# Performance work log

Measured on AMD Instinct MI355X. Metric: run time of the kernel, lower is better.

Reference implementation:

```python
import jax, jax.numpy as jnp
import numpy as np
import math

B, S, HID, H = 2, 2048, 2048, 16
D = HID // H  # head_dim = 128


def rotate_half(x):
    x1, x2 = x[..., : x.shape[-1] // 2], x[..., x.shape[-1] // 2:]
    return jnp.concatenate((-x2, x1), axis=-1)


def setup_inputs() -> dict:
    key = jax.random.key(0)
    ks = jax.random.split(key, 6)
    x = jax.random.normal(ks[0], (B, S, HID), dtype=jnp.float32)
    # learned projection weights (torch Linear: y = x @ W.T); store as [in, out]
    scale = 1.0 / math.sqrt(HID)
    Wq = jax.random.normal(ks[1], (HID, HID), dtype=jnp.float32) * scale
    Wk = jax.random.normal(ks[2], (HID, HID), dtype=jnp.float32) * scale
    Wv = jax.random.normal(ks[3], (HID, HID), dtype=jnp.float32) * scale
    Wo = jax.random.normal(ks[4], (HID, HID), dtype=jnp.float32) * scale
    # causal additive mask [1,1,S,S]
    causal = jnp.tril(jnp.ones((S, S), dtype=bool))
    attention_mask = jnp.where(causal, 0.0, -1e9).astype(jnp.float32)[None, None]
    # ALiBi bias: slope per head times key position, broadcast over queries
    slopes = 2.0 ** (-8.0 * (jnp.arange(1, H + 1, dtype=jnp.float32) / H))
    alibi = (-slopes[:, None] * jnp.arange(S, dtype=jnp.float32)[None, :])[None, :, None, :]  # [1,H,1,S]
    # RoPE tables broadcastable to [B,H,S,D]
    inv_freq = 1.0 / (10000.0 ** (jnp.arange(0, D // 2, dtype=jnp.float32) / (D // 2)))
    t = jnp.arange(S, dtype=jnp.float32)
    freqs = t[:, None] * inv_freq[None, :]            # [S, D/2]
    emb = jnp.concatenate((freqs, freqs), axis=-1)    # [S, D]
    freqs_cos = jnp.cos(emb)[None, None]              # [1,1,S,D]
    freqs_sin = jnp.sin(emb)[None, None]
    return {"x": x, "Wq": Wq, "Wk": Wk, "Wv": Wv, "Wo": Wo,
            "attention_mask": attention_mask, "alibi": alibi,
            "freqs_cos": freqs_cos, "freqs_sin": freqs_sin}


def reference(x, Wq, Wk, Wv, Wo, attention_mask, alibi, freqs_cos, freqs_sin):
    b, s, _ = x.shape
    def split_heads(y):
        return y.reshape(b, s, H, D).transpose(0, 2, 1, 3)  # [B,H,S,D]
    q = split_heads(x @ Wq)
    k = split_heads(x @ Wk)
    v = split_heads(x @ Wv)
    q = q * freqs_cos + rotate_half(q) * freqs_sin
    k = k * freqs_cos + rotate_half(k) * freqs_sin
    scores = jnp.einsum('bhqd,bhkd->bhqk', q, k) / math.sqrt(D)
    scores = scores + attention_mask + alibi
    attn = jax.nn.softmax(scores, axis=-1)  # dropout p=0 (eval) -> identity
    out = jnp.einsum('bhqk,bhkd->bhqd', attn, v)
    out = out.transpose(0, 2, 1, 3).reshape(b, s, HID)
    return out @ Wo
```

## Files before the change

kernel.cpp:

```cpp
#include <hip/hip_runtime.h>

#define S_LEN   2048
#define HEADS   16
#define HID_DIM 2048
#define HEAD_D  128
#define BATCH   2

typedef __bf16          bf16x8 __attribute__((ext_vector_type(8)));
typedef unsigned short  u16x8  __attribute__((ext_vector_type(8)));
typedef unsigned short  u16x4  __attribute__((ext_vector_type(4)));
typedef float           f32x4  __attribute__((ext_vector_type(4)));

__device__ __forceinline__ unsigned short f2bf(float f) {
  unsigned u = __builtin_bit_cast(unsigned, f);
  u += 0x7FFFu + ((u >> 16) & 1u);
  return (unsigned short)(u >> 16);
}
__device__ __forceinline__ float bf2f(unsigned short s) {
  unsigned u = ((unsigned)s) << 16;
  return __builtin_bit_cast(float, u);
}

__device__ __forceinline__ f32x4 mfma16(u16x8 a, u16x8 b, f32x4 c) {
  return __builtin_amdgcn_mfma_f32_16x16x32_bf16(
      __builtin_bit_cast(bf16x8, a), __builtin_bit_cast(bf16x8, b), c, 0, 0, 0);
}

__device__ __forceinline__ void async_load16(const void* g, void* l) {
  __builtin_amdgcn_global_load_lds(
      (const __attribute__((address_space(1))) void*)g,
      (__attribute__((address_space(3))) void*)l, 16, 0, 0);
}

__global__ __launch_bounds__(256) void cvt_bf16(const float* __restrict__ in,
                                                unsigned short* __restrict__ out,
                                                int n8) {
  for (int i = blockIdx.x * blockDim.x + threadIdx.x; i < n8;
       i += gridDim.x * blockDim.x) {
    const float4* p = (const float4*)in + 2L * i;
    float4 a = p[0], b = p[1];
    u16x8 v;
    v[0] = f2bf(a.x); v[1] = f2bf(a.y); v[2] = f2bf(a.z); v[3] = f2bf(a.w);
    v[4] = f2bf(b.x); v[5] = f2bf(b.y); v[6] = f2bf(b.z); v[7] = f2bf(b.w);
    ((u16x8*)out)[i] = v;
  }
}

__global__ __launch_bounds__(256) void transpose_cvt3(
    const float* __restrict__ W0, const float* __restrict__ W1,
    const float* __restrict__ W2, unsigned short* __restrict__ O0,
    unsigned short* __restrict__ O1, unsigned short* __restrict__ O2,
    int dim) {
  __shared__ float tile[32][33];
  const int z = blockIdx.z;
  const float* W = (z == 0) ? W0 : (z == 1) ? W1 : W2;
  unsigned short* Wt = (z == 0) ? O0 : (z == 1) ? O1 : O2;
  const int bx = blockIdx.x * 32, by = blockIdx.y * 32;
  const int tx = threadIdx.x, ty = threadIdx.y;
#pragma unroll
  for (int i = 0; i < 32; i += 8)
    tile[ty + i][tx] = W[(long)(by + ty + i) * dim + bx + tx];
  __syncthreads();
#pragma unroll
  for (int i = 0; i < 32; i += 8)
    Wt[(long)(bx + ty + i) * dim + by + tx] = f2bf(tile[tx][ty + i]);
}

__global__ __launch_bounds__(256) void transpose_cvt(const float* __restrict__ W,
                                                     unsigned short* __restrict__ Wt,
                                                     int dim) {
  __shared__ float tile[32][33];
  const int bx = blockIdx.x * 32, by = blockIdx.y * 32;
  const int tx = threadIdx.x, ty = threadIdx.y;
#pragma unroll
  for (int i = 0; i < 32; i += 8)
    tile[ty + i][tx] = W[(long)(by + ty + i) * dim + bx + tx];
  __syncthreads();
#pragma unroll
  for (int i = 0; i < 32; i += 8)
    Wt[(long)(bx + ty + i) * dim + by + tx] = f2bf(tile[tx][ty + i]);
}

__global__ __launch_bounds__(256) void transpose_v(const unsigned short* __restrict__ V,
                                                   unsigned short* __restrict__ Vt) {
  __shared__ unsigned short tile[32][34];
  const int s0 = blockIdx.x * 32, d0 = blockIdx.y * 32, bh = blockIdx.z;
  const int b = bh >> 4, h = bh & 15;
  const int tx = threadIdx.x, ty = threadIdx.y;
#pragma unroll
  for (int i = 0; i < 32; i += 8)
    tile[ty + i][tx] =
        V[(long)(b * S_LEN + s0 + ty + i) * HID_DIM + h * HEAD_D + d0 + tx];
  __syncthreads();
#pragma unroll
  for (int i = 0; i < 32; i += 8)
    Vt[((long)bh * HEAD_D + d0 + ty + i) * S_LEN + s0 + tx] = tile[tx][ty + i];
}

__global__ __launch_bounds__(256) void rope_qk(unsigned short* __restrict__ Qb,
                                               unsigned short* __restrict__ Kb,
                                               const float* __restrict__ fcos,
                                               const float* __restrict__ fsin) {
  const long i = (long)blockIdx.x * blockDim.x + threadIdx.x;
  const int d = (int)(i & 63);
  const int h = (int)((i >> 6) & (HEADS - 1));
  const long row = i >> 10;
  const int s = (int)(row & (S_LEN - 1));
  const long base = row * HID_DIM + h * HEAD_D + d;
  const float c0 = fcos[s * HEAD_D + d], c1 = fcos[s * HEAD_D + d + 64];
  const float s0 = fsin[s * HEAD_D + d], s1 = fsin[s * HEAD_D + d + 64];
  const float q0 = bf2f(Qb[base]), q1 = bf2f(Qb[base + 64]);
  Qb[base]      = f2bf(q0 * c0 - q1 * s0);
  Qb[base + 64] = f2bf(q1 * c1 + q0 * s1);
  const float k0 = bf2f(Kb[base]), k1 = bf2f(Kb[base + 64]);
  Kb[base]      = f2bf(k0 * c0 - k1 * s0);
  Kb[base + 64] = f2bf(k1 * c1 + k0 * s1);
}

template <int BM>
__global__ __launch_bounds__(512, 2) void gemm9(
    const unsigned short* __restrict__ A,
    const unsigned short* __restrict__ Bt0,
    unsigned short* __restrict__ Cb0,
    float* __restrict__ Cf,
    int M, int N, int K, long zsB, long zsC) {
  constexpr int MF = BM / 32;
  constexpr int AR = BM / 128;
  constexpr int TR = AR + 2;
  __shared__ __align__(16) unsigned short Abuf[4][BM * 32];
  __shared__ __align__(16) unsigned short Bbuf[4][256 * 32];
  const int t = threadIdx.x;
  const int lane = t & 63;
  const int w = t >> 6;
  const int wr = w >> 2, wc = w & 3;
  const int l15 = lane & 15, l4 = lane >> 4;

  const int nwg = gridDim.x;
  const int bid = blockIdx.x;
  const int sw = (bid & 7) * (nwg >> 3) + (bid >> 3);
  const int nbx = N >> 8, nby = M / BM;
  const int z = sw / (nbx * nby);
  const int rem = sw - z * nbx * nby;
  const int by = rem / nbx;
  const int bx = rem - by * nbx;

  const unsigned short* Bt = Bt0 + (long)z * zsB;
  unsigned short* Cb = Cb0 ? Cb0 + (long)z * zsC : nullptr;

  f32x4 acc[MF][4] = {};

  const int kcol = 8 * ((t & 3) ^ ((t >> 3) & 3));
  const unsigned short* aSrc = A + ((long)by * BM + (t >> 2)) * K + kcol;
  const unsigned short* bSrc = Bt + ((long)bx * 256 + (t >> 2)) * K + kcol;

  const int swzr = 8 * (l4 ^ ((l15 >> 1) & 3));
  const int aROff = (wr * (BM / 2) + l15) * 32 + swzr;
  const int bROff = (wc * 64 + l15) * 32 + swzr;

  const int NT = K >> 5;

#define STG(slot, kt_) do {                                              \
    _Pragma("unroll")                                                    \
    for (int r_ = 0; r_ < AR; ++r_)                                      \
      async_load16(aSrc + (long)(kt_) * 32 + (long)r_ * 128 * K,         \
                   (char*)(&Abuf[slot][0]) + r_ * 8192 + t * 16);        \
    async_load16(bSrc + (long)(kt_) * 32,                                \
                 (char*)(&Bbuf[slot][0]) + t * 16);                      \
    async_load16(bSrc + (long)(kt_) * 32 + 128L * K,                     \
                 (char*)(&Bbuf[slot][0]) + 8192 + t * 16);               \
  } while (0)

  STG(0, 0);
  STG(1, 1);
  asm volatile("s_waitcnt vmcnt(%0)" ::"n"(TR) : "memory");
  __builtin_amdgcn_s_barrier();

  for (int kt = 0; kt < NT; ++kt) {
    const int slot = kt & 3;
    const unsigned short* Ab = &Abuf[slot][0];
    const unsigned short* Bb = &Bbuf[slot][0];
    const bool stg = (kt + 2) < NT;
    u16x8 af[MF], bfr[4];
#pragma unroll
    for (int n = 0; n < 4; ++n) bfr[n] = *(const u16x8*)&Bb[bROff + n * 512];
#pragma unroll
    for (int m = 0; m < MF; ++m) af[m] = *(const u16x8*)&Ab[aROff + m * 512];
    if (stg) STG((kt + 2) & 3, kt + 2);
    __builtin_amdgcn_s_setprio(1);
#pragma unroll
    for (int m = 0; m < MF; ++m)
#pragma unroll
      for (int n = 0; n < 4; ++n)
        acc[m][n] = mfma16(af[m], bfr[n], acc[m][n]);
    __builtin_amdgcn_s_setprio(0);
    __builtin_amdgcn_sched_barrier(0);
    if (kt + 1 < NT) {
      if (stg) asm volatile("s_waitcnt vmcnt(%0)" ::"n"(TR) : "memory");
      else     asm volatile("s_waitcnt vmcnt(0)" ::: "memory");
      __builtin_amdgcn_s_barrier();
    }
  }
#undef STG

  const long orow = (long)by * BM + wr * (BM / 2) + l4 * 4;
  const long ocol = (long)bx * 256 + wc * 64 + l15;
#pragma unroll
  for (int m = 0; m < MF; ++m)
#pragma unroll
    for (int n = 0; n < 4; ++n)
#pragma unroll
      for (int r = 0; r < 4; ++r) {
        const long row = orow + m * 16 + r;
        const long col = ocol + n * 16;
        if (Cb) Cb[row * N + col] = f2bf(acc[m][n][r]);
        else    Cf[row * N + col] = acc[m][n][r];
      }
}

__global__ __launch_bounds__(256) void attn_fwd5(const unsigned short* __restrict__ Q,
                                                 const unsigned short* __restrict__ K,
                                                 const unsigned short* __restrict__ Vt,
                                                 const float* __restrict__ alibi,
                                                 unsigned short* __restrict__ O) {
  __shared__ __align__(16) unsigned short Kl[2][32 * 128];
  __shared__ __align__(16) unsigned short Vl[2][64 * 64];
  __shared__ __align__(16) unsigned short Pl[4][32][40];
  const int t = threadIdx.x;
  const int lane = t & 63;
  const int w = t >> 6;
  const int l15 = lane & 15, l4 = lane >> 4;

  const int bid = blockIdx.x;
  const int xcd = bid & 7;
  const int idx = bid >> 3;
  const int qh = idx >> 4;
  const int ql = idx & 15;
  const int qt = (qh < 2) ? ql : (15 - ql);
  const int bh = xcd * 4 + qh;
  const int b = bh >> 4, h = bh & 15;
  const int q0b = qt * 128;
  const int q0 = q0b + w * 32;
  const float nslope = alibi[h * S_LEN + 1];
  const float scale = 0.08838834764831845f;

  const long rowbase = ((long)b * S_LEN) * HID_DIM + h * HEAD_D;
  const long vtbase  = ((long)bh * HEAD_D) * S_LEN;

  u16x8 qf[2][4];
  {
    const unsigned short* qp = Q + rowbase + (long)(q0 + l15) * HID_DIM + l4 * 8;
#pragma unroll
    for (int m = 0; m < 2; ++m)
#pragma unroll
      for (int ds = 0; ds < 4; ++ds)
        qf[m][ds] = *(const u16x8*)(qp + (long)m * 16 * HID_DIM + ds * 32);
  }

  f32x4 acc[2][8] = {};
  float m_r[2] = {-1e30f, -1e30f};
  float l_r[2] = {0.f, 0.f};

  int dd, rw, cbl;
  dd = 16 * t;        rw = dd >> 8; cbl = (dd & 255) ^ ((rw & 7) << 4);
  const unsigned short* ksrc0 = K + rowbase + (long)rw * HID_DIM + (cbl >> 1);
  dd = 4096 + 16 * t; rw = dd >> 8; cbl = (dd & 255) ^ ((rw & 7) << 4);
  const unsigned short* ksrc1 = K + rowbase + (long)rw * HID_DIM + (cbl >> 1);
  dd = 16 * t;        rw = dd >> 7; cbl = (dd & 127) ^ ((rw & 3) << 4);
  const unsigned short* vsrc0 =
      Vt + vtbase + (long)(2 * rw + (cbl >> 6)) * S_LEN + ((cbl & 63) >> 1);
  dd = 4096 + 16 * t; rw = dd >> 7; cbl = (dd & 127) ^ ((rw & 3) << 4);
  const unsigned short* vsrc1 =
      Vt + vtbase + (long)(2 * rw + (cbl >> 6)) * S_LEN + ((cbl & 63) >> 1);

#define ASTAGE(buf, kt_) do {                                             \
    const long kadd = (long)(kt_) * 32 * HID_DIM;                         \
    async_load16(ksrc0 + kadd, (char*)(&Kl[buf][0]) + 16 * t);            \
    async_load16(ksrc1 + kadd, (char*)(&Kl[buf][0]) + 4096 + 16 * t);     \
    async_load16(vsrc0 + (kt_) * 32, (char*)(&Vl[buf][0]) + 16 * t);      \
    async_load16(vsrc1 + (kt_) * 32, (char*)(&Vl[buf][0]) + 4096 + 16 * t); \
  } while (0)

  const int ntB = qt * 4 + 4;
  const int mykt = q0 >> 5;

  ASTAGE(0, 0);
  __syncthreads();

  int cur = 0;
  for (int kt = 0; kt < ntB; ++kt) {
    const int kb = kt * 32;
    if (kt + 1 < ntB) ASTAGE(cur ^ 1, kt + 1);
    if (kt <= mykt) {
      const char* Kc = (const char*)&Kl[cur][0];
      const char* Vc = (const char*)&Vl[cur][0];
      f32x4 sacc[2][2] = {};
#pragma unroll
      for (int ds = 0; ds < 4; ++ds) {
        u16x8 kfr[2];
#pragma unroll
        for (int n = 0; n < 2; ++n) {
          const int R = 16 * n + l15;
          const int cb = (ds * 64 + l4 * 16) ^ ((l15 & 7) << 4);
          kfr[n] = *(const u16x8*)(Kc + R * 256 + cb);
        }
#pragma unroll
        for (int n = 0; n < 2; ++n)
#pragma unroll
          for (int m = 0; m < 2; ++m)
            sacc[n][m] = mfma16(kfr[n], qf[m][ds], sacc[n][m]);
      }
#pragma unroll
      for (int m = 0; m < 2; ++m) {
        const int q = q0 + 16 * m + l15;
        float pv[2][4];
        float rmax = -1e30f;
#pragma unroll
        for (int n = 0; n < 2; ++n)
#pragma unroll
          for (int r = 0; r < 4; ++r) {
            const int k = kb + 16 * n + l4 * 4 + r;
            float v = sacc[n][m][r] * scale + nslope * (float)k;
            if (k > q) v = -1e30f;
            pv[n][r] = v;
            rmax = fmaxf(rmax, v);
          }
        rmax = fmaxf(rmax, __shfl_xor(rmax, 16, 64));
        rmax = fmaxf(rmax, __shfl_xor(rmax, 32, 64));
        const float mnew = fmaxf(m_r[m], rmax);
        const float sf = __expf(m_r[m] - mnew);
        m_r[m] = mnew;
        float rsum = 0.f;
#pragma unroll
        for (int n = 0; n < 2; ++n)
#pragma unroll
          for (int r = 0; r < 4; ++r) {
            pv[n][r] = __expf(pv[n][r] - mnew);
            rsum += pv[n][r];
          }
        rsum += __shfl_xor(rsum, 16, 64);
        rsum += __shfl_xor(rsum, 32, 64);
        l_r[m] = l_r[m] * sf + rsum;
        float sfo[4];
#pragma unroll
        for (int r = 0; r < 4; ++r) sfo[r] = __shfl(sf, l4 * 4 + r, 64);
#pragma unroll
        for (int dt = 0; dt < 8; ++dt)
#pragma unroll
          for (int r = 0; r < 4; ++r) acc[m][dt][r] *= sfo[r];
#pragma unroll
        for (int n = 0; n < 2; ++n) {
          u16x4 pk;
#pragma unroll
          for (int r = 0; r < 4; ++r) pk[r] = f2bf(pv[n][r]);
          *(u16x4*)&Pl[w][16 * m + l15][16 * n + l4 * 4] = pk;
        }
      }
      u16x8 pf[2];
#pragma unroll
      for (int m = 0; m < 2; ++m)
        pf[m] = *(const u16x8*)&Pl[w][16 * m + l15][l4 * 8];
#pragma unroll
      for (int dt = 0; dt < 8; ++dt) {
        const int d = dt * 16 + l15;
        const int vrow = d >> 1;
        const int cbv = (((d & 1) << 6) | (l4 << 4)) ^ ((vrow & 3) << 4);
        u16x8 vb = *(const u16x8*)(Vc + vrow * 128 + cbv);
#pragma unroll
        for (int m = 0; m < 2; ++m)
          acc[m][dt] = mfma16(pf[m], vb, acc[m][dt]);
      }
    }
    __builtin_amdgcn_sched_barrier(0);
    __syncthreads();
    cur ^= 1;
  }
#undef ASTAGE

#pragma unroll
  for (int m = 0; m < 2; ++m) {
    float linv[4];
#pragma unroll
    for (int r = 0; r < 4; ++r)
      linv[r] = 1.0f / __shfl(l_r[m], l4 * 4 + r, 64);
#pragma unroll
    for (int dt = 0; dt < 8; ++dt)
#pragma unroll
      for (int r = 0; r < 4; ++r) {
        const long row = q0 + 16 * m + l4 * 4 + r;
        O[rowbase + row * HID_DIM + dt * 16 + l15] = f2bf(acc[m][dt][r] * linv[r]);
      }
  }
}

extern "C" void kernel_launch(void* const* d_in, const int* in_sizes, int n_in,
                              void* d_out, int out_size, void* d_ws, size_t ws_size,
                              hipStream_t stream) {
  const float* x    = (const float*)d_in[0];
  const float* Wq   = (const float*)d_in[1];
  const float* Wk   = (const float*)d_in[2];
  const float* Wv   = (const float*)d_in[3];
  const float* Wo   = (const float*)d_in[4];
  const float* alibi = (const float*)d_in[6];
  const float* fcos  = (const float*)d_in[7];
  const float* fsin  = (const float*)d_in[8];

  char* ws = (char*)d_ws;
  unsigned short* xb  = (unsigned short*)(ws);
  unsigned short* wtq = (unsigned short*)(ws + (16L << 20));
  unsigned short* wtk = (unsigned short*)(ws + (24L << 20));
  unsigned short* wtv = (unsigned short*)(ws + (32L << 20));
  unsigned short* VtG = (unsigned short*)(ws + (24L << 20));
  unsigned short* Qb  = (unsigned short*)(ws + (40L << 20));
  unsigned short* Kb  = (unsigned short*)(ws + (56L << 20));
  unsigned short* Vb  = (unsigned short*)(ws + (72L << 20));

  const int M = BATCH * S_LEN;
  const int N = HID_DIM;
  const int K = HID_DIM;

  cvt_bf16<<<2048, 256, 0, stream>>>(x, xb, M * K / 8);

  dim3 tb(32, 8);
  transpose_cvt3<<<dim3(N / 32, K / 32, 3), tb, 0, stream>>>(
      Wq, Wk, Wv, wtq, wtk, wtv, N);

  gemm9<256><<<3 * (M / 256) * (N / 256), 512, 0, stream>>>(
      xb, wtq, Qb, nullptr, M, N, K,
      (long)HID_DIM * HID_DIM, (long)(8 << 20));

  rope_qk<<<(BATCH * S_LEN * HEADS * 64) / 256, 256, 0, stream>>>(Qb, Kb, fcos, fsin);

  transpose_v<<<dim3(S_LEN / 32, HEAD_D / 32, BATCH * HEADS), tb, 0, stream>>>(Vb, VtG);

  transpose_cvt<<<dim3(N / 32, K / 32), tb, 0, stream>>>(Wo, wtq, N);

  attn_fwd5<<<512, 256, 0, stream>>>(Qb, Kb, VtG, alibi, xb);

  gemm9<128><<<(M / 128) * (N / 256), 512, 0, stream>>>(
      xb, wtq, nullptr, (float*)d_out, M, N, K, 0L, 0L);
}
```

Measured before the change: 315.2 us.

## Use 128x128 GEMM tiles with triple buffering, fold softmax scale into RoPE, skip masking off-diagonal

The GEMM is replaced by a 256-thread kernel with 128x128 tiles and a 3-slot LDS ring, replacing the 512-thread 256-wide tiles. The smaller tiles give more blocks and higher occupancy, at the cost of less operand reuse per tile. The 1/sqrt(D) softmax scale moves into the RoPE kernel's Q write, so the attention loop drops one multiply per score. Causal masking is now applied only on the diagonal key tile, and the ALiBi terms are computed once per tile rather than per row.

```diff
diff --git a/kernel.cpp b/kernel.cpp
--- a/kernel.cpp
+++ b/kernel.cpp
@@ -101,6 +101,7 @@
                                                unsigned short* __restrict__ Kb,
                                                const float* __restrict__ fcos,
                                                const float* __restrict__ fsin) {
+  const float SC = 0.08838834764831845f;
   const long i = (long)blockIdx.x * blockDim.x + threadIdx.x;
   const int d = (int)(i & 63);
   const int h = (int)((i >> 6) & (HEADS - 1));
@@ -110,35 +111,31 @@
   const float c0 = fcos[s * HEAD_D + d], c1 = fcos[s * HEAD_D + d + 64];
   const float s0 = fsin[s * HEAD_D + d], s1 = fsin[s * HEAD_D + d + 64];
   const float q0 = bf2f(Qb[base]), q1 = bf2f(Qb[base + 64]);
-  Qb[base]      = f2bf(q0 * c0 - q1 * s0);
-  Qb[base + 64] = f2bf(q1 * c1 + q0 * s1);
+  Qb[base]      = f2bf((q0 * c0 - q1 * s0) * SC);
+  Qb[base + 64] = f2bf((q1 * c1 + q0 * s1) * SC);
   const float k0 = bf2f(Kb[base]), k1 = bf2f(Kb[base + 64]);
   Kb[base]      = f2bf(k0 * c0 - k1 * s0);
   Kb[base + 64] = f2bf(k1 * c1 + k0 * s1);
 }
 
-template <int BM>
-__global__ __launch_bounds__(512, 2) void gemm9(
+__global__ __launch_bounds__(256, 3) void gemm10(
     const unsigned short* __restrict__ A,
     const unsigned short* __restrict__ Bt0,
     unsigned short* __restrict__ Cb0,
     float* __restrict__ Cf,
     int M, int N, int K, long zsB, long zsC) {
-  constexpr int MF = BM / 32;
-  constexpr int AR = BM / 128;
-  constexpr int TR = AR + 2;
-  __shared__ __align__(16) unsigned short Abuf[4][BM * 32];
-  __shared__ __align__(16) unsigned short Bbuf[4][256 * 32];
+  __shared__ __align__(16) unsigned short Abuf[3][128 * 32];
+  __shared__ __align__(16) unsigned short Bbuf[3][128 * 32];
   const int t = threadIdx.x;
   const int lane = t & 63;
   const int w = t >> 6;
-  const int wr = w >> 2, wc = w & 3;
+  const int wr = w >> 1, wc = w & 1;
   const int l15 = lane & 15, l4 = lane >> 4;
 
   const int nwg = gridDim.x;
   const int bid = blockIdx.x;
   const int sw = (bid & 7) * (nwg >> 3) + (bid >> 3);
-  const int nbx = N >> 8, nby = M / BM;
+  const int nbx = N >> 7, nby = M >> 7;
   const int z = sw / (nbx * nby);
   const int rem = sw - z * nbx * nby;
   const int by = rem / nbx;
@@ -147,65 +144,69 @@
   const unsigned short* Bt = Bt0 + (long)z * zsB;
   unsigned short* Cb = Cb0 ? Cb0 + (long)z * zsC : nullptr;
 
-  f32x4 acc[MF][4] = {};
+  f32x4 acc[4][4] = {};
 
   const int kcol = 8 * ((t & 3) ^ ((t >> 3) & 3));
-  const unsigned short* aSrc = A + ((long)by * BM + (t >> 2)) * K + kcol;
-  const unsigned short* bSrc = Bt + ((long)bx * 256 + (t >> 2)) * K + kcol;
+  const unsigned short* aSrc = A + ((long)by * 128 + (t >> 2)) * K + kcol;
+  const unsigned short* bSrc = Bt + ((long)bx * 128 + (t >> 2)) * K + kcol;
 
   const int swzr = 8 * (l4 ^ ((l15 >> 1) & 3));
-  const int aROff = (wr * (BM / 2) + l15) * 32 + swzr;
+  const int aROff = (wr * 64 + l15) * 32 + swzr;
   const int bROff = (wc * 64 + l15) * 32 + swzr;
 
   const int NT = K >> 5;
 
 #define STG(slot, kt_) do {                                              \
-    _Pragma("unroll")                                                    \
-    for (int r_ = 0; r_ < AR; ++r_)                                      \
-      async_load16(aSrc + (long)(kt_) * 32 + (long)r_ * 128 * K,         \
-                   (char*)(&Abuf[slot][0]) + r_ * 8192 + t * 16);        \
+    async_load16(aSrc + (long)(kt_) * 32,                                \
+                 (char*)(&Abuf[slot][0]) + t * 16);                      \
+    async_load16(aSrc + (long)(kt_) * 32 + 64L * K,                      \
+                 (char*)(&Abuf[slot][0]) + 4096 + t * 16);               \
     async_load16(bSrc + (long)(kt_) * 32,                                \
                  (char*)(&Bbuf[slot][0]) + t * 16);                      \
-    async_load16(bSrc + (long)(kt_) * 32 + 128L * K,                     \
-                 (char*)(&Bbuf[slot][0]) + 8192 + t * 16);               \
+    async_load16(bSrc + (long)(kt_) * 32 + 64L * K,                      \
+                 (char*)(&Bbuf[slot][0]) + 4096 + t * 16);               \
   } while (0)
 
   STG(0, 0);
   STG(1, 1);
-  asm volatile("s_waitcnt vmcnt(%0)" ::"n"(TR) : "memory");
+  asm volatile("s_waitcnt vmcnt(4)" ::: "memory");
   __builtin_amdgcn_s_barrier();
 
+  int cur = 0;
   for (int kt = 0; kt < NT; ++kt) {
-    const int slot = kt & 3;
-    const unsigned short* Ab = &Abuf[slot][0];
-    const unsigned short* Bb = &Bbuf[slot][0];
+    const unsigned short* Ab = &Abuf[cur][0];
+    const unsigned short* Bb = &Bbuf[cur][0];
     const bool stg = (kt + 2) < NT;
-    u16x8 af[MF], bfr[4];
+    u16x8 af[4], bfr[4];
 #pragma unroll
     for (int n = 0; n < 4; ++n) bfr[n] = *(const u16x8*)&Bb[bROff + n * 512];
 #pragma unroll
-    for (int m = 0; m < MF; ++m) af[m] = *(const u16x8*)&Ab[aROff + m * 512];
-    if (stg) STG((kt + 2) & 3, kt + 2);
+    for (int m = 0; m < 4; ++m) af[m] = *(const u16x8*)&Ab[aROff + m * 512];
+    if (stg) {
+      const int s2 = (cur + 2 >= 3) ? cur - 1 : cur + 2;
+      STG(s2, kt + 2);
+    }
     __builtin_amdgcn_s_setprio(1);
 #pragma unroll
-    for (int m = 0; m < MF; ++m)
+    for (int m = 0; m < 4; ++m)
 #pragma unroll
       for (int n = 0; n < 4; ++n)
         acc[m][n] = mfma16(af[m], bfr[n], acc[m][n]);
     __builtin_amdgcn_s_setprio(0);
     __builtin_amdgcn_sched_barrier(0);
     if (kt + 1 < NT) {
-      if (stg) asm volatile("s_waitcnt vmcnt(%0)" ::"n"(TR) : "memory");
+      if (stg) asm volatile("s_waitcnt vmcnt(4)" ::: "memory");
       else     asm volatile("s_waitcnt vmcnt(0)" ::: "memory");
       __builtin_amdgcn_s_barrier();
     }
+    cur = (cur + 1 >= 3) ? 0 : cur + 1;
   }
 #undef STG
 
-  const long orow = (long)by * BM + wr * (BM / 2) + l4 * 4;
-  const long ocol = (long)bx * 256 + wc * 64 + l15;
-#pragma unroll
-  for (int m = 0; m < MF; ++m)
+  const long orow = (long)by * 128 + wr * 64 + l4 * 4;
+  const long ocol = (long)bx * 128 + wc * 64 + l15;
+#pragma unroll
+  for (int m = 0; m < 4; ++m)
 #pragma unroll
     for (int n = 0; n < 4; ++n)
 #pragma unroll
@@ -217,7 +218,7 @@
       }
 }
 
-__global__ __launch_bounds__(256) void attn_fwd5(const unsigned short* __restrict__ Q,
+__global__ __launch_bounds__(256) void attn_fwd6(const unsigned short* __restrict__ Q,
                                                  const unsigned short* __restrict__ K,
                                                  const unsigned short* __restrict__ Vt,
                                                  const float* __restrict__ alibi,
@@ -241,7 +242,6 @@
   const int q0b = qt * 128;
   const int q0 = q0b + w * 32;
   const float nslope = alibi[h * S_LEN + 1];
-  const float scale = 0.08838834764831845f;
 
   const long rowbase = ((long)b * S_LEN) * HID_DIM + h * HEAD_D;
   const long vtbase  = ((long)bh * HEAD_D) * S_LEN;
@@ -309,21 +309,39 @@
           for (int m = 0; m < 2; ++m)
             sacc[n][m] = mfma16(kfr[n], qf[m][ds], sacc[n][m]);
       }
+      float ak[2][4];
+#pragma unroll
+      for (int n = 0; n < 2; ++n)
+#pragma unroll
+        for (int r = 0; r < 4; ++r)
+          ak[n][r] = nslope * (float)(kb + 16 * n + l4 * 4 + r);
+      const bool diag = (kt == mykt);
 #pragma unroll
       for (int m = 0; m < 2; ++m) {
         const int q = q0 + 16 * m + l15;
         float pv[2][4];
         float rmax = -1e30f;
-#pragma unroll
-        for (int n = 0; n < 2; ++n)
-#pragma unroll
-          for (int r = 0; r < 4; ++r) {
-            const int k = kb + 16 * n + l4 * 4 + r;
-            float v = sacc[n][m][r] * scale + nslope * (float)k;
-            if (k > q) v = -1e30f;
-            pv[n][r] = v;
-            rmax = fmaxf(rmax, v);
-          }
+        if (!diag) {
+#pragma unroll
+          for (int n = 0; n < 2; ++n)
+#pragma unroll
+            for (int r = 0; r < 4; ++r) {
+              const float v = sacc[n][m][r] + ak[n][r];
+              pv[n][r] = v;
+              rmax = fmaxf(rmax, v);
+            }
+        } else {
+#pragma unroll
+          for (int n = 0; n < 2; ++n)
+#pragma unroll
+            for (int r = 0; r < 4; ++r) {
+              const int k = kb + 16 * n + l4 * 4 + r;
+              float v = sacc[n][m][r] + ak[n][r];
+              if (k > q) v = -1e30f;
+              pv[n][r] = v;
+              rmax = fmaxf(rmax, v);
+            }
+        }
         rmax = fmaxf(rmax, __shfl_xor(rmax, 16, 64));
         rmax = fmaxf(rmax, __shfl_xor(rmax, 32, 64));
         const float mnew = fmaxf(m_r[m], rmax);
@@ -424,7 +442,7 @@
   transpose_cvt3<<<dim3(N / 32, K / 32, 3), tb, 0, stream>>>(
       Wq, Wk, Wv, wtq, wtk, wtv, N);
 
-  gemm9<256><<<3 * (M / 256) * (N / 256), 512, 0, stream>>>(
+  gemm10<<<3 * (M / 128) * (N / 128), 256, 0, stream>>>(
       xb, wtq, Qb, nullptr, M, N, K,
       (long)HID_DIM * HID_DIM, (long)(8 << 20));
 
@@ -434,8 +452,8 @@
 
   transpose_cvt<<<dim3(N / 32, K / 32), tb, 0, stream>>>(Wo, wtq, N);
 
-  attn_fwd5<<<512, 256, 0, stream>>>(Qb, Kb, VtG, alibi, xb);
-
-  gemm9<128><<<(M / 128) * (N / 256), 512, 0, stream>>>(
+  attn_fwd6<<<512, 256, 0, stream>>>(Qb, Kb, VtG, alibi, xb);
+
+  gemm10<<<(M / 128) * (N / 128), 256, 0, stream>>>(
       xb, wtq, nullptr, (float*)d_out, M, N, K, 0L, 0L);
 }
```

New measurement: 365.0 us. 1.16x slower.
